# Optimization experiments

Hardware: AMD Instinct MI355X
Metric: run time of the kernel (lower is better)

Reference implementation:

```python
import jax, jax.numpy as jnp
import numpy as np

S, B, F, H, L = 256, 64, 512, 512, 4
INV_SQRT_H = float(1.0 / np.sqrt(H))


def _ln(x, g, b, eps=1e-5):
    # torch nn.LayerNorm: biased variance, eps=1e-5
    mu = jnp.mean(x, axis=-1, keepdims=True)
    var = jnp.var(x, axis=-1, keepdims=True)
    return (x - mu) * jax.lax.rsqrt(var + eps) * g + b


def setup_inputs() -> dict:
    key = jax.random.key(0)
    k1, k2 = jax.random.split(key)
    x = jax.random.normal(k1, (S, B, F), dtype=jnp.float32)  # time-major [S,B,F]
    W = jax.random.normal(k2, (L, 6, F, H), dtype=jnp.float32) * 0.02  # q,k,v,i,f,o
    b = jnp.zeros((L, 6, H), jnp.float32)
    ln_g = jnp.ones((L, 6, H), jnp.float32)
    ln_b = jnp.zeros((L, 6, H), jnp.float32)
    return {"x": x, "W": W, "b": b, "ln_g": ln_g, "ln_b": ln_b}


def reference(x, W, b, ln_g, ln_b):
    # Dropout is identity (eval mode / p effectively 0).
    def step(carry, x_t):
        h, c, n = carry  # each [L,B,H]
        layer_input = x_t  # [B,F]
        hs, cs, ns = [], [], []
        for l in range(L):
            # all 6 gate projections in one einsum: [6,B,H]
            z = jnp.einsum('bf,gfh->gbh', layer_input, W[l]) + b[l][:, None, :]
            z = z.at[1].multiply(INV_SQRT_H)  # k = Wk(x)/sqrt(H) before LN
            z = _ln(z, ln_g[l][:, None, :], ln_b[l][:, None, :])
            q, k, v = z[0], z[1], z[2]
            i = jax.nn.sigmoid(z[3])
            f = jax.nn.sigmoid(z[4])
            o = jax.nn.sigmoid(z[5])
            # (k[:,:,None] @ v[:,None,:]).sum(dim=1) == k.sum(-1,keepdims)*v
            kv_sum = jnp.sum(k, axis=-1, keepdims=True) * v
            c_l = f * c[l] + i * kv_sum
            n_l = f * n[l] + i * k
            n_hat = n_l / (jnp.linalg.norm(n_l, axis=-1, keepdims=True) + 1e-8)
            h_l = o * jnp.tanh(q * n_hat)
            if l > 0:  # residual_conn
                h_l = h_l + layer_input
            layer_input = h_l
            hs.append(h_l); cs.append(c_l); ns.append(n_l)
        h = jnp.stack(hs); c = jnp.stack(cs); n = jnp.stack(ns)
        return (h, c, n), h[-1]

    init = tuple(jnp.zeros((L, B, H), x.dtype) for _ in range(3))
    (h, c, n), out = jax.lax.scan(step, init, x)  # out: [S,B,H] time-major
    return out, h, c, n
```

## Files before the change

kernel.cpp:

```cpp
#include <hip/hip_runtime.h>


typedef unsigned short u16;
typedef unsigned int   u32;
typedef short s8v  __attribute__((ext_vector_type(8)));
typedef float f16v __attribute__((ext_vector_type(16)));

#define S_    256
#define B_    64
#define F_    512
#define H_    512
#define L_    4
#define NG    3072
#define RALL  16384
#define CH    16
#define INV_SQRT_H 0.044194173824159216f

__device__ __forceinline__ float bu2f(u16 u) {
    union { u32 i; float f; } z; z.i = ((u32)u) << 16; return z.f;
}
__device__ __forceinline__ u16 f2bf(float f) {
    union { float f; u32 i; } z; z.f = f;
    u32 r = (z.i + 0x7FFFu + ((z.i >> 16) & 1u)) >> 16;
    return (u16)r;
}
__device__ __forceinline__ float sigm(float x)  { return 1.0f / (1.0f + __expf(-x)); }
__device__ __forceinline__ float tanhf_(float x){ return 2.0f / (1.0f + __expf(-2.0f * x)) - 1.0f; }
__device__ __forceinline__ float wred64(float v) {
    #pragma unroll
    for (int m = 1; m < 64; m <<= 1) v += __shfl_xor(v, m);
    return v;
}
__device__ __forceinline__ void gl_lds16(const u16* g, u16* l) {
    __builtin_amdgcn_global_load_lds((const __attribute__((address_space(1))) u32*)g,
                                     (__attribute__((address_space(3))) u32*)l, 16, 0, 0);
}
__device__ __forceinline__ void unp8(uint4 u, float* f) {
    f[0] = bu2f((u16)(u.x & 0xffff)); f[1] = bu2f((u16)(u.x >> 16));
    f[2] = bu2f((u16)(u.y & 0xffff)); f[3] = bu2f((u16)(u.y >> 16));
    f[4] = bu2f((u16)(u.z & 0xffff)); f[5] = bu2f((u16)(u.z >> 16));
    f[6] = bu2f((u16)(u.w & 0xffff)); f[7] = bu2f((u16)(u.w >> 16));
}
__device__ __forceinline__ uint4 pck8(const float* f) {
    uint4 u;
    u.x = (u32)f2bf(f[0]) | ((u32)f2bf(f[1]) << 16);
    u.y = (u32)f2bf(f[2]) | ((u32)f2bf(f[3]) << 16);
    u.z = (u32)f2bf(f[4]) | ((u32)f2bf(f[5]) << 16);
    u.w = (u32)f2bf(f[6]) | ((u32)f2bf(f[7]) << 16);
    return u;
}

__global__ void convw_k(const float* __restrict__ W, u16* __restrict__ WT) {
    __shared__ float tile[32][33];
    const int lg = blockIdx.z;
    const int h0 = blockIdx.x * 32, f0 = blockIdx.y * 32;
    const float* Wb = W  + (size_t)lg * F_ * H_;
    u16*        WTb = WT + (size_t)lg * F_ * H_;
    const int tx = threadIdx.x, ty = threadIdx.y;
    #pragma unroll
    for (int i = 0; i < 32; i += 8)
        tile[ty + i][tx] = Wb[(size_t)(f0 + ty + i) * H_ + h0 + tx];
    __syncthreads();
    #pragma unroll
    for (int i = 0; i < 32; i += 8)
        WTb[(size_t)(h0 + ty + i) * F_ + f0 + tx] = f2bf(tile[tx][ty + i]);
}

__global__ void convx_k(const float* __restrict__ x, u16* __restrict__ A) {
    const int i = blockIdx.x * 256 + threadIdx.x;
    float4 v = ((const float4*)x)[i];
    u32 lo = (u32)f2bf(v.x) | ((u32)f2bf(v.y) << 16);
    u32 hi = (u32)f2bf(v.z) | ((u32)f2bf(v.w) << 16);
    ((uint2*)A)[i] = make_uint2(lo, hi);
}

__global__ __launch_bounds__(256) void gemm_k(const u16* __restrict__ A,
                                              const u16* __restrict__ BT,
                                              u16* __restrict__ Z,
                                              const float* __restrict__ bias,
                                              int arow0) {
    __shared__ u16 lsA[128 * 64];
    __shared__ u16 lsB[128 * 64];
    const int t = threadIdx.x;
    const int ntile = blockIdx.x;
    const int mtile = blockIdx.y;
    const int ncol0 = ntile * 128;
    const u16* Ab = A  + (size_t)(arow0 + mtile * 128) * F_;
    const u16* Bb = BT + (size_t)ntile * 128 * F_;
    const int lane = t & 63, wv = t >> 6;

    f16v acc[2][2];
    #pragma unroll
    for (int i = 0; i < 2; i++)
        #pragma unroll
        for (int j = 0; j < 2; j++) acc[i][j] = 0.0f;

    const int wm = (wv >> 1) * 64, wn = (wv & 1) * 64;
    const int rl = lane & 31, hi = lane >> 5;
    const int r7 = rl & 7;

    int goff[4];
    #pragma unroll
    for (int s = 0; s < 4; s++) {
        const int c = t + 256 * s;
        const int row = c >> 3, slot = c & 7;
        const int g = slot ^ (row & 7);
        goff[s] = row * F_ + g * 8;
    }

    for (int kb = 0; kb < 8; ++kb) {
        const int kofs = kb * 64;
        #pragma unroll
        for (int s = 0; s < 4; s++) {
            const int c = t + 256 * s;
            gl_lds16(Ab + goff[s] + kofs, lsA + c * 8);
            gl_lds16(Bb + goff[s] + kofs, lsB + c * 8);
        }
        __syncthreads();
        #pragma unroll
        for (int s = 0; s < 4; ++s) {
            const int slot = ((s << 1) + hi) ^ r7;
            s8v fa[2], fb[2];
            #pragma unroll
            for (int i = 0; i < 2; i++)
                fa[i] = *(const s8v*)(lsA + (wm + i * 32 + rl) * 64 + slot * 8);
            #pragma unroll
            for (int j = 0; j < 2; j++)
                fb[j] = *(const s8v*)(lsB + (wn + j * 32 + rl) * 64 + slot * 8);
            #pragma unroll
            for (int i = 0; i < 2; i++)
                #pragma unroll
                for (int j = 0; j < 2; j++)
                    acc[i][j] = __builtin_amdgcn_mfma_f32_32x32x16_bf16(fa[i], fb[j], acc[i][j], 0, 0, 0);
        }
        __syncthreads();
    }

    #pragma unroll
    for (int j = 0; j < 2; j++) {
        const int col = ncol0 + wn + j * 32 + rl;
        const float bv = bias[col];
        #pragma unroll
        for (int i = 0; i < 2; i++) {
            const int mbase = mtile * 128 + wm + i * 32 + hi * 4;
            #pragma unroll
            for (int reg = 0; reg < 16; reg++) {
                const int row = mbase + (reg & 3) + 8 * (reg >> 2);
                Z[(size_t)row * NG + col] = f2bf(acc[i][j][reg] + bv);
            }
        }
    }
}

__global__ __launch_bounds__(256) void stats_k(const u16* __restrict__ Z,
                                               const float* __restrict__ lng1,
                                               const float* __restrict__ lnb1,
                                               float* __restrict__ stats) {
    const int wid = threadIdx.x >> 6, lane = threadIdx.x & 63;
    const int row = blockIdx.x * 4 + wid;
    const u16* zr = Z + (size_t)row * NG + lane * 8;

    float g1v[8], b1v[8];
    #pragma unroll
    for (int j = 0; j < 8; j++) { g1v[j] = lng1[lane * 8 + j]; b1v[j] = lnb1[lane * 8 + j]; }

    float s[4], sq[4], wk = 0.f, sg1 = 0.f, sb1 = 0.f;
    #pragma unroll
    for (int g = 0; g < 4; ++g) {
        uint4 u = *(const uint4*)(zr + (g + 1) * 512);
        float f[8];
        unp8(u, f);
        float ls = 0.f, lq = 0.f;
        #pragma unroll
        for (int j = 0; j < 8; j++) { ls += f[j]; lq += f[j] * f[j]; }
        s[g] = ls; sq[g] = lq;
        if (g == 0) {
            #pragma unroll
            for (int j = 0; j < 8; j++) wk += g1v[j] * f[j];
        }
    }
    #pragma unroll
    for (int j = 0; j < 8; j++) { sg1 += g1v[j]; sb1 += b1v[j]; }

    #pragma unroll
    for (int g = 0; g < 4; ++g) { s[g] = wred64(s[g]); sq[g] = wred64(sq[g]); }
    wk = wred64(wk); sg1 = wred64(sg1); sb1 = wred64(sb1);

    if (lane == 0) {
        float* o = stats + (size_t)row * 16;
        const float inv = 1.0f / 512.0f;
        float mu1 = 0.f, rs1 = 0.f;
        #pragma unroll
        for (int g = 0; g < 4; ++g) {
            float m = s[g] * inv, e2 = sq[g] * inv;
            if (g == 0) { m *= INV_SQRT_H; e2 *= INV_SQRT_H * INV_SQRT_H; }
            const float rs = rsqrtf(fmaxf(e2 - m * m, 0.0f) + 1e-5f);
            o[1 + g] = m; o[7 + g] = rs;
            if (g == 0) { mu1 = m; rs1 = rs; }
        }
        o[12] = rs1 * (INV_SQRT_H * wk - mu1 * sg1) + sb1;
    }
}

__global__ __launch_bounds__(128) void scanA_k(const u16* __restrict__ Z,
                                               const float* __restrict__ stats,
                                               const float* __restrict__ lngl,
                                               const float* __restrict__ lnbl,
                                               u16* __restrict__ nbuf,
                                               u16* __restrict__ pbuf,
                                               float* __restrict__ sumP,
                                               float* __restrict__ sumC,
                                               float* __restrict__ sumN) {
    const int b = blockIdx.y, chunk = blockIdx.z;
    const int h = blockIdx.x * 128 + threadIdx.x;
    __shared__ float sst[CH][16];
    for (int i = threadIdx.x; i < CH * 16; i += 128) {
        const int tc = i >> 4, j = i & 15;
        sst[tc][j] = stats[(size_t)((chunk * CH + tc) * 64 + b) * 16 + j];
    }
    float gg[4], gb[4];
    #pragma unroll
    for (int g = 0; g < 4; ++g) {
        gg[g] = lngl[(g + 1) * 512 + h];
        gb[g] = lnbl[(g + 1) * 512 + h];
    }
    __syncthreads();

    float c = 0.f, n = 0.f, P = 1.f;
    #pragma unroll 4
    for (int tc = 0; tc < CH; ++tc) {
        const int r = (chunk * CH + tc) * 64 + b;
        const u16* zr = Z + (size_t)r * NG + h;
        const float z1 = bu2f(zr[512]);
        const float z2 = bu2f(zr[1024]);
        const float z3 = bu2f(zr[1536]);
        const float z4 = bu2f(zr[2048]);
        const float kk = (z1 * INV_SQRT_H - sst[tc][1]) * sst[tc][7] * gg[0] + gb[0];
        const float vv = (z2 - sst[tc][2]) * sst[tc][8]  * gg[1] + gb[1];
        const float ii = sigm((z3 - sst[tc][3]) * sst[tc][9]  * gg[2] + gb[2]);
        const float ff = sigm((z4 - sst[tc][4]) * sst[tc][10] * gg[3] + gb[3]);
        c = ff * c + ii * (sst[tc][12] * vv);
        n = ff * n + ii * kk;
        P *= ff;
        nbuf[(size_t)r * 512 + h] = f2bf(n);
        pbuf[(size_t)r * 512 + h] = f2bf(P);
    }
    const size_t idx = ((size_t)chunk << 15) + (b << 9) + h;
    sumP[idx] = P; sumC[idx] = c; sumN[idx] = n;
}

__global__ __launch_bounds__(256) void scanB_k(const float* __restrict__ sumP,
                                               const float* __restrict__ sumC,
                                               const float* __restrict__ sumN,
                                               float* __restrict__ n0buf,
                                               float* __restrict__ cstate,
                                               float* __restrict__ nstate,
                                               float* __restrict__ finals,
                                               int t0, int NC, int l) {
    const int idx = blockIdx.x * 256 + threadIdx.x;
    float c, n;
    if (t0 == 0) { c = 0.f; n = 0.f; }
    else { c = cstate[idx]; n = nstate[idx]; }
    for (int ch = 0; ch < NC; ++ch) {
        const size_t o = ((size_t)ch << 15) + idx;
        n0buf[o] = n;
        const float P = sumP[o];
        c = sumC[o] + P * c;
        n = sumN[o] + P * n;
    }
    if (t0 + NC * CH == S_) {
        const int b = idx >> 9, h = idx & 511;
        const size_t so = ((size_t)l * B_ + b) * H_ + h;
        finals[(size_t)L_ * B_ * H_ + so] = c;
        finals[(size_t)2 * L_ * B_ * H_ + so] = n;
    } else {
        cstate[idx] = c; nstate[idx] = n;
    }
}

__global__ __launch_bounds__(256) void normh_k(const u16* __restrict__ Z,
                                               const u16* __restrict__ nbuf,
                                               const u16* __restrict__ pbuf,
                                               const float* __restrict__ n0buf,
                                               const float* __restrict__ lngl,
                                               const float* __restrict__ lnbl,
                                               float* __restrict__ hbuf,
                                               u16* __restrict__ aoutB,
                                               float* __restrict__ outp,
                                               float* __restrict__ finals,
                                               int t0, int l) {
    const int wid = threadIdx.x >> 6, lane = threadIdx.x & 63;
    const int r = blockIdx.x * 4 + wid;
    const int h0 = lane * 8;

    float nl[8], pv[8];
    unp8(*(const uint4*)(nbuf + (size_t)r * 512 + h0), nl);
    unp8(*(const uint4*)(pbuf + (size_t)r * 512 + h0), pv);
    const float* n0r = n0buf + ((size_t)(r >> 10) << 15) + ((size_t)(r & 63) << 9) + h0;
    const float4 na = *(const float4*)(n0r);
    const float4 nb = *(const float4*)(n0r + 4);
    const float n0v[8] = {na.x, na.y, na.z, na.w, nb.x, nb.y, nb.z, nb.w};

    const u16* zr = Z + (size_t)r * NG;
    float z0[8], z5[8];
    unp8(*(const uint4*)(zr + h0), z0);
    unp8(*(const uint4*)(zr + 2560 + h0), z5);

    float nsq = 0.f, s0 = 0.f, q0 = 0.f, s5 = 0.f, q5 = 0.f;
    float nv[8];
    #pragma unroll
    for (int j = 0; j < 8; j++) {
        nv[j] = fmaf(pv[j], n0v[j], nl[j]);
        nsq += nv[j] * nv[j];
        s0 += z0[j]; q0 += z0[j] * z0[j];
        s5 += z5[j]; q5 += z5[j] * z5[j];
    }
    nsq = wred64(nsq);
    s0 = wred64(s0); q0 = wred64(q0);
    s5 = wred64(s5); q5 = wred64(q5);
    const float rinv = 1.0f / (sqrtf(nsq) + 1e-8f);
    const float inv = 1.0f / 512.0f;
    const float mu0 = s0 * inv, mu5 = s5 * inv;
    const float rs0 = rsqrtf(fmaxf(q0 * inv - mu0 * mu0, 0.0f) + 1e-5f);
    const float rs5 = rsqrtf(fmaxf(q5 * inv - mu5 * mu5, 0.0f) + 1e-5f);

    float g0[8], b0[8], g5[8], b5[8];
    #pragma unroll
    for (int j = 0; j < 8; j++) {
        g0[j] = lngl[h0 + j];        b0[j] = lnbl[h0 + j];
        g5[j] = lngl[2560 + h0 + j]; b5[j] = lnbl[2560 + h0 + j];
    }

    const int tl = r >> 6, b = r & 63;
    const int gr = t0 + tl;
    const size_t grow = (((size_t)gr * 64 + b) * 512) + h0;

    float hv[8];
    #pragma unroll
    for (int j = 0; j < 8; j++) {
        const float q  = (z0[j] - mu0) * rs0 * g0[j] + b0[j];
        const float oo = sigm((z5[j] - mu5) * rs5 * g5[j] + b5[j]);
        hv[j] = oo * tanhf_(q * nv[j] * rinv);
    }
    if (l > 0) {
        #pragma unroll
        for (int j = 0; j < 8; j++) hv[j] += hbuf[grow + j];
    }
    if (outp) {
        #pragma unroll
        for (int j = 0; j < 8; j++) outp[grow + j] = hv[j];
    } else {
        #pragma unroll
        for (int j = 0; j < 8; j++) hbuf[grow + j] = hv[j];
    }
    if (aoutB) *(uint4*)(aoutB + grow) = pck8(hv);

    if (gr == S_ - 1) {
        const size_t so = (((size_t)l * B_ + b) * 512) + h0;
        #pragma unroll
        for (int j = 0; j < 8; j++) finals[so + j] = hv[j];
    }
}

extern "C" void kernel_launch(void* const* d_in, const int* in_sizes, int n_in,
                              void* d_out, int out_size, void* d_ws, size_t ws_size,
                              hipStream_t stream) {
    const float* x   = (const float*)d_in[0];
    const float* W   = (const float*)d_in[1];
    const float* bia = (const float*)d_in[2];
    const float* lng = (const float*)d_in[3];
    const float* lnb = (const float*)d_in[4];
    float* out = (float*)d_out;

    const size_t WT_B = (size_t)L_ * 6 * H_ * F_ * 2;
    const size_t A_B  = (size_t)RALL * F_ * 2;
    const size_t ST_B = (size_t)RALL * 16 * 4;
    const size_t CS_B = (size_t)B_ * H_ * 4;
    const size_t HB_B = (size_t)RALL * H_ * 4;
    auto zB  = [](int T) { return (size_t)T * B_ * NG * 2; };
    auto nB  = [](int T) { return (size_t)T * B_ * H_ * 2; };
    auto cxB = [](int T) { return (size_t)(T / CH) * B_ * H_ * 4; };
    const size_t base = WT_B + A_B + ST_B + 2 * CS_B + HB_B + 32768;

    int T = 16;
    const int cand[3] = {256, 64, 16};
    for (int i = 0; i < 3; i++) {
        const int Tc = cand[i];
        if (ws_size >= base + zB(Tc) + 2 * nB(Tc) + 4 * cxB(Tc)) { T = Tc; break; }
    }
    const int NC = T / CH;

    char* ws = (char*)d_ws;
    size_t off = 0;
    auto take = [&](size_t nb) { size_t o = off; off += (nb + 255) & ~(size_t)255; return o; };
    u16*   WT    = (u16*)  (ws + take(WT_B));
    u16*   Abf   = (u16*)  (ws + take(A_B));
    float* stats = (float*)(ws + take(ST_B));
    float* cs    = (float*)(ws + take(CS_B));
    float* ns    = (float*)(ws + take(CS_B));
    float* hbuf  = (float*)(ws + take(HB_B));
    u16*   zb    = (u16*)  (ws + take(zB(T)));
    u16*   nbuf  = (u16*)  (ws + take(nB(T)));
    u16*   pbuf  = (u16*)  (ws + take(nB(T)));
    float* sumP  = (float*)(ws + take(cxB(T)));
    float* sumC  = (float*)(ws + take(cxB(T)));
    float* sumN  = (float*)(ws + take(cxB(T)));
    float* n0buf = (float*)(ws + take(cxB(T)));

    convw_k<<<dim3(16, 16, 24), dim3(32, 8), 0, stream>>>(W, WT);
    convx_k<<<dim3(RALL * F_ / 4 / 256), dim3(256), 0, stream>>>(x, Abf);

    float* finals = out + (size_t)S_ * B_ * H_;
    for (int l = 0; l < L_; ++l) {
        const u16*   WTl   = WT  + (size_t)l * 6 * H_ * F_;
        const float* biasl = bia + (size_t)l * NG;
        const float* lngl  = lng + (size_t)l * 6 * H_;
        const float* lnbl  = lnb + (size_t)l * 6 * H_;
        for (int j = 0; j < S_ / T; ++j) {
            const int t0 = j * T, arow0 = t0 * B_;
            const int rows = T * B_;
            gemm_k<<<dim3(24, rows / 128), dim3(256), 0, stream>>>(Abf, WTl, zb, biasl, arow0);
            stats_k<<<dim3(rows / 4), dim3(256), 0, stream>>>(zb, lngl + H_, lnbl + H_, stats);
            scanA_k<<<dim3(4, B_, NC), dim3(128), 0, stream>>>(zb, stats, lngl, lnbl,
                                                               nbuf, pbuf, sumP, sumC, sumN);
            scanB_k<<<dim3(128), dim3(256), 0, stream>>>(sumP, sumC, sumN, n0buf,
                                                         cs, ns, finals, t0, NC, l);
            normh_k<<<dim3(rows / 4), dim3(256), 0, stream>>>(zb, nbuf, pbuf, n0buf,
                                                              lngl, lnbl, hbuf,
                                                              (l < 3) ? Abf : (u16*)nullptr,
                                                              (l == 3) ? out : (float*)nullptr,
                                                              finals, t0, l);
        }
    }
}
```

Baseline: 605.9 us.

## Rewrite gate GEMM as 256x256 double-buffered MFMA pipeline with XCD-aware tile swizzle

The projection GEMM moves from 128x128 tiles with 256 threads and a single LDS buffer to 256x256 tiles with 512 threads. LDS is double-buffered so global-to-LDS loads for the next k-step are issued while the current one is computed. It uses 16x16x32 MFMA with explicit barriers, waitcnt and setprio interleaving, and remaps block IDs so neighbouring tiles land on the same XCD. The goal is to hide load latency and raise operand reuse in the GEMM. In exchange it uses more registers and LDS per block, launches fewer blocks per chunk, and adds fragile hand-placed synchronisation. The grid size assumes the row count is a multiple of 256 and the block count a multiple of 8.

```diff
diff --git a/kernel.cpp b/kernel.cpp
--- a/kernel.cpp
+++ b/kernel.cpp
@@ -3,8 +3,8 @@
 
 typedef unsigned short u16;
 typedef unsigned int   u32;
-typedef short s8v  __attribute__((ext_vector_type(8)));
-typedef float f16v __attribute__((ext_vector_type(16)));
+typedef short s8v __attribute__((ext_vector_type(8)));
+typedef float f4v __attribute__((ext_vector_type(4)));
 
 #define S_    256
 #define B_    64
@@ -74,80 +74,154 @@
     ((uint2*)A)[i] = make_uint2(lo, hi);
 }
 
-__global__ __launch_bounds__(256) void gemm_k(const u16* __restrict__ A,
-                                              const u16* __restrict__ BT,
-                                              u16* __restrict__ Z,
-                                              const float* __restrict__ bias,
-                                              int arow0) {
-    __shared__ u16 lsA[128 * 64];
-    __shared__ u16 lsB[128 * 64];
+__global__ __launch_bounds__(512, 2) void gemm_k(const u16* __restrict__ A,
+                                                 const u16* __restrict__ BT,
+                                                 u16* __restrict__ Z,
+                                                 const float* __restrict__ bias,
+                                                 int arow0) {
+    __shared__ __align__(16) u16 lsA[2][2][16][512];
+    __shared__ __align__(16) u16 lsB[2][2][16][512];
+
+    const int bid = blockIdx.x, nwg = gridDim.x;
+    const int cpx = nwg >> 3;
+    const int swz = (bid & 7) * cpx + (bid >> 3);
+    const int ntile = swz % 12, mtile = swz / 12;
+    const int ncol0 = ntile * 256;
+
     const int t = threadIdx.x;
-    const int ntile = blockIdx.x;
-    const int mtile = blockIdx.y;
-    const int ncol0 = ntile * 128;
-    const u16* Ab = A  + (size_t)(arow0 + mtile * 128) * F_;
-    const u16* Bb = BT + (size_t)ntile * 128 * F_;
     const int lane = t & 63, wv = t >> 6;
-
-    f16v acc[2][2];
-    #pragma unroll
-    for (int i = 0; i < 2; i++)
-        #pragma unroll
-        for (int j = 0; j < 2; j++) acc[i][j] = 0.0f;
-
-    const int wm = (wv >> 1) * 64, wn = (wv & 1) * 64;
-    const int rl = lane & 31, hi = lane >> 5;
-    const int r7 = rl & 7;
-
-    int goff[4];
-    #pragma unroll
-    for (int s = 0; s < 4; s++) {
-        const int c = t + 256 * s;
-        const int row = c >> 3, slot = c & 7;
-        const int g = slot ^ (row & 7);
-        goff[s] = row * F_ + g * 8;
-    }
-
-    for (int kb = 0; kb < 8; ++kb) {
-        const int kofs = kb * 64;
-        #pragma unroll
-        for (int s = 0; s < 4; s++) {
-            const int c = t + 256 * s;
-            gl_lds16(Ab + goff[s] + kofs, lsA + c * 8);
-            gl_lds16(Bb + goff[s] + kofs, lsB + c * 8);
-        }
-        __syncthreads();
-        #pragma unroll
-        for (int s = 0; s < 4; ++s) {
-            const int slot = ((s << 1) + hi) ^ r7;
-            s8v fa[2], fb[2];
+    const int l15 = lane & 15, l4 = lane >> 4;
+    const int lane8 = lane << 3;
+    const int wm = (wv >> 2) * 8;
+    const int wn = (wv & 3) * 4;
+
+    const u16* Ab  = A  + (size_t)(arow0 + mtile * 256) * F_;
+    const u16* Bb  = BT + (size_t)ncol0 * F_;
+    const u16* gA0 = Ab + (size_t)(wv * 16 + l15) * F_ + l4 * 8;
+    const u16* gA1 = gA0 + (size_t)128 * F_;
+    const u16* gB0 = Bb + (size_t)(wv * 16 + l15) * F_ + l4 * 8;
+    const u16* gB1 = gB0 + (size_t)128 * F_;
+
+    f4v acc[8][4];
+    #pragma unroll
+    for (int m = 0; m < 8; ++m)
+        #pragma unroll
+        for (int n = 0; n < 4; ++n) acc[m][n] = 0.0f;
+
+    auto stA = [&](int db, int ks, int kb) {
+        const int ko = kb * 64 + ks * 32;
+        gl_lds16(gA0 + ko, &lsA[db][ks][wv][lane8]);
+        gl_lds16(gA1 + ko, &lsA[db][ks][8 + wv][lane8]);
+    };
+    auto stB = [&](int db, int ks, int kb) {
+        const int ko = kb * 64 + ks * 32;
+        gl_lds16(gB0 + ko, &lsB[db][ks][wv][lane8]);
+        gl_lds16(gB1 + ko, &lsB[db][ks][8 + wv][lane8]);
+    };
+
+    stA(0, 0, 0); stB(0, 0, 0); stA(0, 1, 0); stB(0, 1, 0);
+    asm volatile("s_waitcnt vmcnt(4)" ::: "memory");
+    __builtin_amdgcn_s_barrier();
+    asm volatile("" ::: "memory");
+
+    s8v fa[8], fb[2];
+    #pragma unroll 2
+    for (int kt = 0; kt < 8; ++kt) {
+        const int d = kt & 1, dn = d ^ 1;
+        const int kn = (kt < 7) ? kt + 1 : 7;
+
+        #pragma unroll
+        for (int m = 0; m < 8; ++m) fa[m] = *(const s8v*)&lsA[d][0][wm + m][lane8];
+        fb[0] = *(const s8v*)&lsB[d][0][wn + 0][lane8];
+        fb[1] = *(const s8v*)&lsB[d][0][wn + 1][lane8];
+        stA(dn, 0, kn);
+        asm volatile("" ::: "memory");
+        __builtin_amdgcn_s_barrier();
+        asm volatile("s_waitcnt lgkmcnt(0)" ::: "memory");
+        __builtin_amdgcn_sched_barrier(0);
+        __builtin_amdgcn_s_setprio(1);
+        #pragma unroll
+        for (int m = 0; m < 8; ++m) {
+            acc[m][0] = __builtin_amdgcn_mfma_f32_16x16x32_bf16(fa[m], fb[0], acc[m][0], 0, 0, 0);
+            acc[m][1] = __builtin_amdgcn_mfma_f32_16x16x32_bf16(fa[m], fb[1], acc[m][1], 0, 0, 0);
+        }
+        __builtin_amdgcn_s_setprio(0);
+        asm volatile("" ::: "memory");
+        __builtin_amdgcn_s_barrier();
+        asm volatile("" ::: "memory");
+
+        fb[0] = *(const s8v*)&lsB[d][0][wn + 2][lane8];
+        fb[1] = *(const s8v*)&lsB[d][0][wn + 3][lane8];
+        stB(dn, 0, kn);
+        asm volatile("" ::: "memory");
+        __builtin_amdgcn_s_barrier();
+        asm volatile("s_waitcnt lgkmcnt(0)" ::: "memory");
+        __builtin_amdgcn_sched_barrier(0);
+        __builtin_amdgcn_s_setprio(1);
+        #pragma unroll
+        for (int m = 0; m < 8; ++m) {
+            acc[m][2] = __builtin_amdgcn_mfma_f32_16x16x32_bf16(fa[m], fb[0], acc[m][2], 0, 0, 0);
+            acc[m][3] = __builtin_amdgcn_mfma_f32_16x16x32_bf16(fa[m], fb[1], acc[m][3], 0, 0, 0);
+        }
+        __builtin_amdgcn_s_setprio(0);
+        asm volatile("s_waitcnt vmcnt(4)" ::: "memory");
+        __builtin_amdgcn_s_barrier();
+        asm volatile("" ::: "memory");
+
+        #pragma unroll
+        for (int m = 0; m < 8; ++m) fa[m] = *(const s8v*)&lsA[d][1][wm + m][lane8];
+        fb[0] = *(const s8v*)&lsB[d][1][wn + 0][lane8];
+        fb[1] = *(const s8v*)&lsB[d][1][wn + 1][lane8];
+        stA(dn, 1, kn);
+        asm volatile("" ::: "memory");
+        __builtin_amdgcn_s_barrier();
+        asm volatile("s_waitcnt lgkmcnt(0)" ::: "memory");
+        __builtin_amdgcn_sched_barrier(0);
+        __builtin_amdgcn_s_setprio(1);
+        #pragma unroll
+        for (int m = 0; m < 8; ++m) {
+            acc[m][0] = __builtin_amdgcn_mfma_f32_16x16x32_bf16(fa[m], fb[0], acc[m][0], 0, 0, 0);
+            acc[m][1] = __builtin_amdgcn_mfma_f32_16x16x32_bf16(fa[m], fb[1], acc[m][1], 0, 0, 0);
+        }
+        __builtin_amdgcn_s_setprio(0);
+        asm volatile("" ::: "memory");
+        __builtin_amdgcn_s_barrier();
+        asm volatile("" ::: "memory");
+
+        fb[0] = *(const s8v*)&lsB[d][1][wn + 2][lane8];
+        fb[1] = *(const s8v*)&lsB[d][1][wn + 3][lane8];
+        stB(dn, 1, kn);
+        asm volatile("" ::: "memory");
+        __builtin_amdgcn_s_barrier();
+        asm volatile("s_waitcnt lgkmcnt(0)" ::: "memory");
+        __builtin_amdgcn_sched_barrier(0);
+        __builtin_amdgcn_s_setprio(1);
+        #pragma unroll
+        for (int m = 0; m < 8; ++m) {
+            acc[m][2] = __builtin_amdgcn_mfma_f32_16x16x32_bf16(fa[m], fb[0], acc[m][2], 0, 0, 0);
+            acc[m][3] = __builtin_amdgcn_mfma_f32_16x16x32_bf16(fa[m], fb[1], acc[m][3], 0, 0, 0);
+        }
+        __builtin_amdgcn_s_setprio(0);
+        asm volatile("s_waitcnt vmcnt(4)" ::: "memory");
+        __builtin_amdgcn_s_barrier();
+        asm volatile("" ::: "memory");
+    }
+
+    asm volatile("s_waitcnt vmcnt(0)" ::: "memory");
+
+    const int rb0 = mtile * 256 + (wv >> 2) * 128 + l4 * 4;
+    const int cb0 = ncol0 + (wv & 3) * 64 + l15;
+    #pragma unroll
+    for (int n = 0; n < 4; ++n) {
+        const int col = cb0 + n * 16;
+        const float bv = bias[col];
+        #pragma unroll
+        for (int m = 0; m < 8; ++m) {
+            const int row = rb0 + m * 16;
+            u16* zp = Z + (size_t)row * NG + col;
             #pragma unroll
-            for (int i = 0; i < 2; i++)
-                fa[i] = *(const s8v*)(lsA + (wm + i * 32 + rl) * 64 + slot * 8);
-            #pragma unroll
-            for (int j = 0; j < 2; j++)
-                fb[j] = *(const s8v*)(lsB + (wn + j * 32 + rl) * 64 + slot * 8);
-            #pragma unroll
-            for (int i = 0; i < 2; i++)
-                #pragma unroll
-                for (int j = 0; j < 2; j++)
-                    acc[i][j] = __builtin_amdgcn_mfma_f32_32x32x16_bf16(fa[i], fb[j], acc[i][j], 0, 0, 0);
-        }
-        __syncthreads();
-    }
-
-    #pragma unroll
-    for (int j = 0; j < 2; j++) {
-        const int col = ncol0 + wn + j * 32 + rl;
-        const float bv = bias[col];
-        #pragma unroll
-        for (int i = 0; i < 2; i++) {
-            const int mbase = mtile * 128 + wm + i * 32 + hi * 4;
-            #pragma unroll
-            for (int reg = 0; reg < 16; reg++) {
-                const int row = mbase + (reg & 3) + 8 * (reg >> 2);
-                Z[(size_t)row * NG + col] = f2bf(acc[i][j][reg] + bv);
-            }
+            for (int r = 0; r < 4; ++r)
+                zp[(size_t)r * NG] = f2bf(acc[m][n][r] + bv);
         }
     }
 }
@@ -419,7 +493,7 @@
         for (int j = 0; j < S_ / T; ++j) {
             const int t0 = j * T, arow0 = t0 * B_;
             const int rows = T * B_;
-            gemm_k<<<dim3(24, rows / 128), dim3(256), 0, stream>>>(Abf, WTl, zb, biasl, arow0);
+            gemm_k<<<dim3(12 * (rows / 256)), dim3(512), 0, stream>>>(Abf, WTl, zb, biasl, arow0);
             stats_k<<<dim3(rows / 4), dim3(256), 0, stream>>>(zb, lngl + H_, lnbl + H_, stats);
             scanA_k<<<dim3(4, B_, NC), dim3(128), 0, stream>>>(zb, stats, lngl, lnbl,
                                                                nbuf, pbuf, sumP, sumC, sumN);
```

Result: slower. 741.0 us (+22.3%).

## Restructure GEMM LDS layout, swizzle block order, and stage epilogue through shared memory

Applied to the files above, without the earlier changes.

The GEMM kernel now loads A/B tiles into shared memory in an MFMA-fragment-native layout (each lane's 16-byte chunk placed contiguously per fragment), which removes the XOR slot swizzle and index math. The grid is flattened to 1D with an 8-way block remap so that neighbouring workgroups share tiles, which is meant to improve L2 reuse. The epilogue writes bf16 results into padded shared memory first and then stores 16-byte coalesced rows to Z instead of scattered 2-byte stores. Launch bounds request 4 blocks per CU, which risks register pressure.

```diff
diff --git a/kernel.cpp b/kernel.cpp
--- a/kernel.cpp
+++ b/kernel.cpp
@@ -74,20 +74,31 @@
     ((uint2*)A)[i] = make_uint2(lo, hi);
 }
 
-__global__ __launch_bounds__(256) void gemm_k(const u16* __restrict__ A,
-                                              const u16* __restrict__ BT,
-                                              u16* __restrict__ Z,
-                                              const float* __restrict__ bias,
-                                              int arow0) {
-    __shared__ u16 lsA[128 * 64];
-    __shared__ u16 lsB[128 * 64];
+__global__ __launch_bounds__(256, 4) void gemm_k(const u16* __restrict__ A,
+                                                 const u16* __restrict__ BT,
+                                                 u16* __restrict__ Z,
+                                                 const float* __restrict__ bias,
+                                                 int arow0) {
+    __shared__ __align__(16) u16 ls[17408];
+
+    const int bid = blockIdx.x, nwg = gridDim.x;
+    const int cpx = nwg >> 3;
+    const int swz = (bid & 7) * cpx + (bid >> 3);
+    const int ntile = swz % 24, mtile = swz / 24;
+    const int ncol0 = ntile * 128;
+
     const int t = threadIdx.x;
-    const int ntile = blockIdx.x;
-    const int mtile = blockIdx.y;
-    const int ncol0 = ntile * 128;
+    const int lane = t & 63, wv = t >> 6;
+    const int rl = lane & 31, hi = lane >> 5;
+    const int wm = (wv >> 1) * 64, wn = (wv & 1) * 64;
+    const int fA0 = (wv >> 1) * 2, fB0 = (wv & 1) * 2;
+
     const u16* Ab = A  + (size_t)(arow0 + mtile * 128) * F_;
-    const u16* Bb = BT + (size_t)ntile * 128 * F_;
-    const int lane = t & 63, wv = t >> 6;
+    const u16* Bb = BT + (size_t)ncol0 * F_;
+    const u16* gA = Ab + (size_t)(wv * 32 + rl) * F_ + hi * 8;
+    const u16* gB = Bb + (size_t)(wv * 32 + rl) * F_ + hi * 8;
+    u16* lA = ls + wv * 512 + lane * 8;
+    u16* lB = ls + 8192 + wv * 512 + lane * 8;
 
     f16v acc[2][2];
     #pragma unroll
@@ -95,38 +106,23 @@
         #pragma unroll
         for (int j = 0; j < 2; j++) acc[i][j] = 0.0f;
 
-    const int wm = (wv >> 1) * 64, wn = (wv & 1) * 64;
-    const int rl = lane & 31, hi = lane >> 5;
-    const int r7 = rl & 7;
-
-    int goff[4];
-    #pragma unroll
-    for (int s = 0; s < 4; s++) {
-        const int c = t + 256 * s;
-        const int row = c >> 3, slot = c & 7;
-        const int g = slot ^ (row & 7);
-        goff[s] = row * F_ + g * 8;
-    }
-
     for (int kb = 0; kb < 8; ++kb) {
-        const int kofs = kb * 64;
-        #pragma unroll
-        for (int s = 0; s < 4; s++) {
-            const int c = t + 256 * s;
-            gl_lds16(Ab + goff[s] + kofs, lsA + c * 8);
-            gl_lds16(Bb + goff[s] + kofs, lsB + c * 8);
+        const int ko = kb * 64;
+        #pragma unroll
+        for (int ks = 0; ks < 4; ++ks) {
+            gl_lds16(gA + ko + ks * 16, lA + ks * 2048);
+            gl_lds16(gB + ko + ks * 16, lB + ks * 2048);
         }
         __syncthreads();
         #pragma unroll
-        for (int s = 0; s < 4; ++s) {
-            const int slot = ((s << 1) + hi) ^ r7;
+        for (int ks = 0; ks < 4; ++ks) {
             s8v fa[2], fb[2];
             #pragma unroll
             for (int i = 0; i < 2; i++)
-                fa[i] = *(const s8v*)(lsA + (wm + i * 32 + rl) * 64 + slot * 8);
+                fa[i] = *(const s8v*)(ls + ks * 2048 + (fA0 + i) * 512 + lane * 8);
             #pragma unroll
             for (int j = 0; j < 2; j++)
-                fb[j] = *(const s8v*)(lsB + (wn + j * 32 + rl) * 64 + slot * 8);
+                fb[j] = *(const s8v*)(ls + 8192 + ks * 2048 + (fB0 + j) * 512 + lane * 8);
             #pragma unroll
             for (int i = 0; i < 2; i++)
                 #pragma unroll
@@ -137,17 +133,29 @@
     }
 
     #pragma unroll
-    for (int j = 0; j < 2; j++) {
-        const int col = ncol0 + wn + j * 32 + rl;
-        const float bv = bias[col];
-        #pragma unroll
-        for (int i = 0; i < 2; i++) {
-            const int mbase = mtile * 128 + wm + i * 32 + hi * 4;
+    for (int j = 0; j < 2; ++j) {
+        const int colL = wn + j * 32 + rl;
+        const float bv = bias[ncol0 + colL];
+        #pragma unroll
+        for (int i = 0; i < 2; ++i) {
+            const int rb = wm + i * 32 + hi * 4;
             #pragma unroll
-            for (int reg = 0; reg < 16; reg++) {
-                const int row = mbase + (reg & 3) + 8 * (reg >> 2);
-                Z[(size_t)row * NG + col] = f2bf(acc[i][j][reg] + bv);
+            for (int reg = 0; reg < 16; ++reg) {
+                const int row = rb + (reg & 3) + 8 * (reg >> 2);
+                ls[row * 136 + colL] = f2bf(acc[i][j][reg] + bv);
             }
+        }
+    }
+    __syncthreads();
+    {
+        const int r0 = wv * 32 + (lane >> 4);
+        const int c8 = (lane & 15) * 8;
+        u16* zb_ = Z + (size_t)(mtile * 128) * NG + ncol0;
+        #pragma unroll
+        for (int s = 0; s < 8; ++s) {
+            const int row = r0 + s * 4;
+            const uint4 v = *(const uint4*)(ls + row * 136 + c8);
+            *(uint4*)(zb_ + (size_t)row * NG + c8) = v;
         }
     }
 }
@@ -419,7 +427,7 @@
         for (int j = 0; j < S_ / T; ++j) {
             const int t0 = j * T, arow0 = t0 * B_;
             const int rows = T * B_;
-            gemm_k<<<dim3(24, rows / 128), dim3(256), 0, stream>>>(Abf, WTl, zb, biasl, arow0);
+            gemm_k<<<dim3(24 * (rows / 128)), dim3(256), 0, stream>>>(Abf, WTl, zb, biasl, arow0);
             stats_k<<<dim3(rows / 4), dim3(256), 0, stream>>>(zb, lngl + H_, lnbl + H_, stats);
             scanA_k<<<dim3(4, B_, NC), dim3(128), 0, stream>>>(zb, stats, lngl, lnbl,
                                                                nbuf, pbuf, sumP, sumC, sumN);
```

After: 774.0 us. +27.7%, slower.

## Rewrite GEMM as 256x256 double-buffered pipelined tile with XCD-aware block swizzle

Applied to the files above, without the earlier changes.

The projection GEMM moves from 128x128 tiles with 256 threads and a single LDS buffer to 256x256 tiles with 512 threads (8 waves) and double-buffered LDS. Global-to-LDS loads for the next k-step are issued in phases interleaved with the MFMA work, using manual waitcnt/barriers and setprio. Block IDs are remapped across the 8 XCDs to improve L2 reuse. The larger tile cuts operand re-reads but halves the number of blocks, and the hand-written synchronisation is fragile and could reduce occupancy.

```diff
diff --git a/kernel.cpp b/kernel.cpp
--- a/kernel.cpp
+++ b/kernel.cpp
@@ -74,79 +74,118 @@
     ((uint2*)A)[i] = make_uint2(lo, hi);
 }
 
-__global__ __launch_bounds__(256) void gemm_k(const u16* __restrict__ A,
-                                              const u16* __restrict__ BT,
-                                              u16* __restrict__ Z,
-                                              const float* __restrict__ bias,
-                                              int arow0) {
-    __shared__ u16 lsA[128 * 64];
-    __shared__ u16 lsB[128 * 64];
+__global__ __launch_bounds__(512, 2) void gemm_k(const u16* __restrict__ A,
+                                                 const u16* __restrict__ BT,
+                                                 u16* __restrict__ Z,
+                                                 const float* __restrict__ bias,
+                                                 int arow0) {
+    __shared__ __align__(16) u16 lsA[2][16384];
+    __shared__ __align__(16) u16 lsB[2][16384];
+
+    const int bid = blockIdx.x, nwg = gridDim.x;
+    const int cpx = nwg >> 3;
+    const int swz = (bid & 7) * cpx + (bid >> 3);
+    const int ntile = swz % 12, mtile = swz / 12;
+    const int ncol0 = ntile * 256;
+
     const int t = threadIdx.x;
-    const int ntile = blockIdx.x;
-    const int mtile = blockIdx.y;
-    const int ncol0 = ntile * 128;
-    const u16* Ab = A  + (size_t)(arow0 + mtile * 128) * F_;
-    const u16* Bb = BT + (size_t)ntile * 128 * F_;
     const int lane = t & 63, wv = t >> 6;
-
-    f16v acc[2][2];
-    #pragma unroll
-    for (int i = 0; i < 2; i++)
-        #pragma unroll
-        for (int j = 0; j < 2; j++) acc[i][j] = 0.0f;
-
-    const int wm = (wv >> 1) * 64, wn = (wv & 1) * 64;
     const int rl = lane & 31, hi = lane >> 5;
-    const int r7 = rl & 7;
-
-    int goff[4];
-    #pragma unroll
-    for (int s = 0; s < 4; s++) {
-        const int c = t + 256 * s;
-        const int row = c >> 3, slot = c & 7;
-        const int g = slot ^ (row & 7);
-        goff[s] = row * F_ + g * 8;
-    }
-
-    for (int kb = 0; kb < 8; ++kb) {
-        const int kofs = kb * 64;
-        #pragma unroll
-        for (int s = 0; s < 4; s++) {
-            const int c = t + 256 * s;
-            gl_lds16(Ab + goff[s] + kofs, lsA + c * 8);
-            gl_lds16(Bb + goff[s] + kofs, lsB + c * 8);
-        }
-        __syncthreads();
-        #pragma unroll
-        for (int s = 0; s < 4; ++s) {
-            const int slot = ((s << 1) + hi) ^ r7;
-            s8v fa[2], fb[2];
+    const int wm = (wv >> 2) * 128;
+    const int wn = (wv & 3) * 64;
+
+    const u16* Ab = A  + (size_t)(arow0 + mtile * 256) * F_;
+    const u16* Bb = BT + (size_t)ncol0 * F_;
+
+    int goff[2], loff[2];
+    #pragma unroll
+    for (int u = 0; u < 2; ++u) {
+        const int c2 = t + 512 * u;
+        const int row = c2 >> 2, slot = c2 & 3;
+        const int g = slot ^ ((row >> 1) & 3);
+        goff[u] = row * F_ + g * 8;
+        loff[u] = c2 * 8;
+    }
+
+    f16v acc[4][2];
+    #pragma unroll
+    for (int m = 0; m < 4; ++m)
+        #pragma unroll
+        for (int n = 0; n < 2; ++n) acc[m][n] = 0.0f;
+
+    auto stA = [&](int db, int kh, int kb) {
+        #pragma unroll
+        for (int u = 0; u < 2; ++u)
+            gl_lds16(Ab + goff[u] + kb * 64 + kh * 32, &lsA[db][kh * 8192 + loff[u]]);
+    };
+    auto stB = [&](int db, int kh, int kb) {
+        #pragma unroll
+        for (int u = 0; u < 2; ++u)
+            gl_lds16(Bb + goff[u] + kb * 64 + kh * 32, &lsB[db][kh * 8192 + loff[u]]);
+    };
+
+    stA(0, 0, 0); stB(0, 0, 0); stA(0, 1, 0); stB(0, 1, 0);
+    asm volatile("s_waitcnt vmcnt(4)" ::: "memory");
+    __builtin_amdgcn_s_barrier();
+    asm volatile("" ::: "memory");
+
+    auto phase = [&](int d, int dn, int ks, int kn, bool stageA, bool vmw) {
+        const int kh = ks >> 1;
+        const int kc = 2 * (ks & 1) + hi;
+        s8v fa[4], fb[2];
+        #pragma unroll
+        for (int m = 0; m < 4; ++m) {
+            const int r = wm + m * 32 + rl;
+            const int s4 = kc ^ ((r >> 1) & 3);
+            fa[m] = *(const s8v*)&lsA[d][kh * 8192 + r * 32 + s4 * 8];
+        }
+        #pragma unroll
+        for (int n = 0; n < 2; ++n) {
+            const int r = wn + n * 32 + rl;
+            const int s4 = kc ^ ((r >> 1) & 3);
+            fb[n] = *(const s8v*)&lsB[d][kh * 8192 + r * 32 + s4 * 8];
+        }
+        if (stageA) stA(dn, ks >> 1, kn); else stB(dn, ks >> 1, kn);
+        asm volatile("" ::: "memory");
+        __builtin_amdgcn_s_barrier();
+        asm volatile("s_waitcnt lgkmcnt(0)" ::: "memory");
+        __builtin_amdgcn_sched_barrier(0);
+        __builtin_amdgcn_s_setprio(1);
+        #pragma unroll
+        for (int m = 0; m < 4; ++m)
             #pragma unroll
-            for (int i = 0; i < 2; i++)
-                fa[i] = *(const s8v*)(lsA + (wm + i * 32 + rl) * 64 + slot * 8);
+            for (int n = 0; n < 2; ++n)
+                acc[m][n] = __builtin_amdgcn_mfma_f32_32x32x16_bf16(fa[m], fb[n], acc[m][n], 0, 0, 0);
+        __builtin_amdgcn_s_setprio(0);
+        if (vmw) asm volatile("s_waitcnt vmcnt(4)" ::: "memory");
+        asm volatile("" ::: "memory");
+        __builtin_amdgcn_s_barrier();
+        asm volatile("" ::: "memory");
+    };
+
+    #pragma unroll 2
+    for (int kt = 0; kt < 8; ++kt) {
+        const int d = kt & 1, dn = d ^ 1;
+        const int kn = (kt < 7) ? kt + 1 : 7;
+        phase(d, dn, 0, kn, true,  false);
+        phase(d, dn, 1, kn, false, true);
+        phase(d, dn, 2, kn, true,  false);
+        phase(d, dn, 3, kn, false, true);
+    }
+
+    asm volatile("s_waitcnt vmcnt(0)" ::: "memory");
+
+    #pragma unroll
+    for (int n = 0; n < 2; ++n) {
+        const int col = ncol0 + wn + n * 32 + rl;
+        const float bv = bias[col];
+        #pragma unroll
+        for (int m = 0; m < 4; ++m) {
+            const int mbase = mtile * 256 + wm + m * 32 + hi * 4;
             #pragma unroll
-            for (int j = 0; j < 2; j++)
-                fb[j] = *(const s8v*)(lsB + (wn + j * 32 + rl) * 64 + slot * 8);
-            #pragma unroll
-            for (int i = 0; i < 2; i++)
-                #pragma unroll
-                for (int j = 0; j < 2; j++)
-                    acc[i][j] = __builtin_amdgcn_mfma_f32_32x32x16_bf16(fa[i], fb[j], acc[i][j], 0, 0, 0);
-        }
-        __syncthreads();
-    }
-
-    #pragma unroll
-    for (int j = 0; j < 2; j++) {
-        const int col = ncol0 + wn + j * 32 + rl;
-        const float bv = bias[col];
-        #pragma unroll
-        for (int i = 0; i < 2; i++) {
-            const int mbase = mtile * 128 + wm + i * 32 + hi * 4;
-            #pragma unroll
-            for (int reg = 0; reg < 16; reg++) {
+            for (int reg = 0; reg < 16; ++reg) {
                 const int row = mbase + (reg & 3) + 8 * (reg >> 2);
-                Z[(size_t)row * NG + col] = f2bf(acc[i][j][reg] + bv);
+                Z[(size_t)row * NG + col] = f2bf(acc[m][n][reg] + bv);
             }
         }
     }
@@ -419,7 +458,7 @@
         for (int j = 0; j < S_ / T; ++j) {
             const int t0 = j * T, arow0 = t0 * B_;
             const int rows = T * B_;
-            gemm_k<<<dim3(24, rows / 128), dim3(256), 0, stream>>>(Abf, WTl, zb, biasl, arow0);
+            gemm_k<<<dim3(12 * (rows / 256)), dim3(512), 0, stream>>>(Abf, WTl, zb, biasl, arow0);
             stats_k<<<dim3(rows / 4), dim3(256), 0, stream>>>(zb, lngl + H_, lnbl + H_, stats);
             scanA_k<<<dim3(4, B_, NC), dim3(128), 0, stream>>>(zb, stats, lngl, lnbl,
                                                                nbuf, pbuf, sumP, sumC, sumN);
```

Result: slower. 663.7 us (+9.5%).
